# Optimization experiments

Hardware: AMD Instinct MI355X
Metric: run time of the kernel (lower is better)

The kernel has to match this reference:

```python
import jax, jax.numpy as jnp
import numpy as np

BN_EPS = 1e-5
N_SH, N_SS, N_HH, D = 1195, 390, 805, 64


def _gcn(x, edge_index, W, b, n_nodes, mean):
    # per-edge message = Linear(x_j); lin(x)[src] == lin(x[src])
    h = x @ W + b                                   # [N, out]
    msg = h[edge_index[0]]                          # gather sources -> [E, out]
    agg = jax.ops.segment_sum(msg, edge_index[1], num_segments=n_nodes)
    if mean:
        cnt = jax.ops.segment_sum(jnp.ones((edge_index.shape[1],), x.dtype),
                                  edge_index[1], num_segments=n_nodes)
        agg = agg / jnp.maximum(cnt, 1.0)[:, None]
    return jnp.tanh(agg)


def _bn(x, gamma, beta):
    # BatchNorm1d in training mode: biased batch statistics
    m = jnp.mean(x, axis=0)
    v = jnp.var(x, axis=0)
    return (x - m) * jax.lax.rsqrt(v + BN_EPS) * gamma + beta


def setup_inputs() -> dict:
    key = jax.random.key(0)
    ks = jax.random.split(key, 40)
    f32 = jnp.float32

    def lin(k, din, dout):
        k1, k2 = jax.random.split(k)
        s = 1.0 / np.sqrt(din)
        W = jax.random.uniform(k1, (din, dout), f32, -s, s)
        b = jax.random.uniform(k2, (dout,), f32, -s, s)
        return W, b

    inp = {}
    inp["x_SH"] = jnp.arange(N_SH, dtype=jnp.int64 if jax.config.jax_enable_x64 else jnp.int32)
    inp["edge_index_SH"] = jax.random.randint(ks[0], (2, 1_000_000), 0, N_SH)
    inp["x_SS"] = jnp.arange(N_SS)
    inp["edge_index_SS"] = jax.random.randint(ks[1], (2, 200_000), 0, N_SS)
    inp["x_HH"] = jnp.arange(N_HH)
    inp["edge_index_HH"] = jax.random.randint(ks[2], (2, 200_000), 0, N_HH)
    inp["prescription"] = jax.random.uniform(ks[3], (20000, N_SS), f32)
    inp["kgOneHot"] = jax.random.uniform(ks[4], (N_HH, 27), f32)

    inp["emb"] = jax.random.normal(ks[5], (N_SH, D), f32)
    inp["w_sh1"], inp["b_sh1"] = lin(ks[6], D, D)
    inp["w_sh2"], inp["b_sh2"] = lin(ks[7], D, D)
    inp["w_mlp1"], inp["b_mlp1"] = lin(ks[8], D, 256)
    inp["g_bn1"] = jnp.ones((256,), f32); inp["be_bn1"] = jnp.zeros((256,), f32)
    inp["w_sh1h"], inp["b_sh1h"] = lin(ks[9], D, D)
    inp["w_sh2h"], inp["b_sh2h"] = lin(ks[10], D, D)
    inp["w_mlp1h"], inp["b_mlp1h"] = lin(ks[11], D, 256)
    inp["g_bn1h"] = jnp.ones((256,), f32); inp["be_bn1h"] = jnp.zeros((256,), f32)
    inp["w_ss"], inp["b_ss"] = lin(ks[12], D, 256)
    inp["w_hh"], inp["b_hh"] = lin(ks[13], D + 27, 256)
    inp["w_mlp"], inp["b_mlp"] = lin(ks[14], 256, 256)
    inp["g_si"] = jnp.ones((256,), f32); inp["be_si"] = jnp.zeros((256,), f32)
    return inp


def reference(x_SH, edge_index_SH, x_SS, edge_index_SS, x_HH, edge_index_HH,
              prescription, kgOneHot, emb,
              w_sh1, b_sh1, w_sh2, b_sh2, w_mlp1, b_mlp1, g_bn1, be_bn1,
              w_sh1h, b_sh1h, w_sh2h, b_sh2h, w_mlp1h, b_mlp1h, g_bn1h, be_bn1h,
              w_ss, b_ss, w_hh, b_hh, w_mlp, b_mlp, g_si, be_si):
    # symptom branch on SH graph (mean aggregation)
    x1 = emb[x_SH]                                           # [1195, 64]
    x2 = _gcn(x1, edge_index_SH, w_sh1, b_sh1, N_SH, mean=True)
    x6 = _gcn(x2, edge_index_SH, w_sh2, b_sh2, N_SH, mean=True)
    x9 = (x1 + x2 + x6) / 3.0
    x9 = jnp.tanh(_bn(x9 @ w_mlp1 + b_mlp1, g_bn1, be_bn1))  # [1195, 256]

    # herb branch on SH graph
    x22 = _gcn(x1, edge_index_SH, w_sh1h, b_sh1h, N_SH, mean=True)
    x66 = _gcn(x22, edge_index_SH, w_sh2h, b_sh2h, N_SH, mean=True)
    x99 = (x1 + x22 + x66) / 3.0
    x99 = jnp.tanh(_bn(x99 @ w_mlp1h + b_mlp1h, g_bn1h, be_bn1h))

    # SS graph (add aggregation)
    x_ss1 = _gcn(emb[x_SS], edge_index_SS, w_ss, b_ss, N_SS, mean=False)  # [390, 256]

    # HH graph with KG one-hot features appended
    x_hh0 = jnp.concatenate([emb[x_HH], kgOneHot], axis=-1)  # [805, 91]
    x_hh1 = _gcn(x_hh0, edge_index_HH, w_hh, b_hh, N_HH, mean=False)      # [805, 256]

    es = x9[:N_SS] + x_ss1                                   # [390, 256]
    eh = x99[N_SS:] + x_hh1                                  # [805, 256]

    e_synd = prescription @ es                               # [B, 256]
    pre_sum = jnp.sum(prescription, axis=1, keepdims=True)
    e = e_synd / pre_sum
    e = jax.nn.relu(_bn(e @ w_mlp + b_mlp, g_si, be_si))
    return e @ eh.T                                          # [B, 805]
```

## Files before the change

kernel.cpp:

```cpp
#include <hip/hip_runtime.h>
#include <cstddef>
#include <cstdint>

#define N_SH 1195
#define N_SS 390
#define N_HH 805
#define DIM  64

typedef __bf16 bf16_t;
typedef bf16_t bf16x4v __attribute__((ext_vector_type(4)));
typedef bf16_t bf16x8v __attribute__((ext_vector_type(8)));
typedef float f32x4 __attribute__((ext_vector_type(4)));

__device__ inline ushort f2bf(float f) {
    union { float f; uint32_t u; } c; c.f = f;
    uint32_t u = c.u;
    u += 0x7FFFu + ((u >> 16) & 1u);
    return (ushort)(u >> 16);
}

__device__ inline void xcd_swizzle(int gx, int gy, int& bx, int& by) {
    int nwg = gx * gy;
    int lin = by * gx + bx;
    int q = nwg >> 3, r = nwg & 7;
    int xcd = lin & 7, idx = lin >> 3;
    int nt = (xcd < r ? xcd * (q + 1) : r * (q + 1) + (xcd - r) * q) + idx;
    by = nt / gx; bx = nt % gx;
}

__global__ void build_adj3_kernel(
    const int* __restrict__ e1, int E1, int hs1, uint32_t* __restrict__ T1,
    const int* __restrict__ e2, int E2, int hs2, uint32_t* __restrict__ T2,
    const int* __restrict__ e3, int E3, int hs3, uint32_t* __restrict__ T3)
{
    int i = blockIdx.x * blockDim.x + threadIdx.x;
    if (i < E1) {
        int src = e1[i], dst = e1[E1 + i];
        atomicAdd(&T1[(size_t)dst * hs1 + (src >> 2)], 1u << ((src & 3) * 8));
    } else if (i < E1 + E2) {
        int j = i - E1;
        int src = e2[j], dst = e2[E2 + j];
        atomicAdd(&T2[(size_t)dst * hs2 + (src >> 2)], 1u << ((src & 3) * 8));
    } else if (i < E1 + E2 + E3) {
        int j = i - E1 - E2;
        int src = e3[j], dst = e3[E3 + j];
        atomicAdd(&T3[(size_t)dst * hs3 + (src >> 2)], 1u << ((src & 3) * 8));
    }
}

__global__ void rowsum_inv_packed_kernel(const uint32_t* __restrict__ T, int R,
                                         int halfStride, float* __restrict__ inv) {
    int row  = blockIdx.x * (blockDim.x / 64) + (threadIdx.x / 64);
    int lane = threadIdx.x & 63;
    if (row >= R) return;
    const uint32_t* p = T + (size_t)row * halfStride;
    uint32_t s = 0;
    for (int c = lane; c < halfStride; c += 64) {
        uint32_t w = p[c];
        s += (w & 0xFFu) + ((w >> 8) & 0xFFu) + ((w >> 16) & 0xFFu) + (w >> 24);
    }
    for (int off = 32; off > 0; off >>= 1) s += __shfl_down(s, off);
    if (lane == 0) inv[row] = 1.0f / fmaxf((float)s, 1.0f);
}

__device__ inline void unpack_one(const uint32_t* __restrict__ T, int R, int C,
                                  int hs, ushort* __restrict__ out, int Cp, int i) {
    int r = i / Cp, c = i % Cp;
    float v = 0.f;
    if (r < R && c < C) {
        uint32_t w = T[(size_t)r * hs + (c >> 2)];
        v = (float)((w >> ((c & 3) * 8)) & 0xFFu);
    }
    out[i] = f2bf(v);
}

__global__ void cvt_unpack3_kernel(
    const uint32_t* __restrict__ T1, int hs1, ushort* __restrict__ o1, int n1, int Cp1,
    const uint32_t* __restrict__ T2, int hs2, ushort* __restrict__ o2, int n2, int Cp2,
    const uint32_t* __restrict__ T3, int hs3, ushort* __restrict__ o3, int n3, int Cp3)
{
    int i = blockIdx.x * blockDim.x + threadIdx.x;
    if (i < n1) { unpack_one(T1, N_SH, N_SH, hs1, o1, Cp1, i); return; }
    i -= n1;
    if (i < n2) { unpack_one(T2, N_SS, N_SS, hs2, o2, Cp2, i); return; }
    i -= n2;
    if (i < n3) { unpack_one(T3, N_HH, N_HH, hs3, o3, Cp3, i); }
}

#define BM 64
#define BN 64
#define BK 16

__global__ __launch_bounds__(256) void gemm_kernel(
    const float* __restrict__ A, const float* __restrict__ A2, int ldaA, int ldaA2,
    const float* __restrict__ B,
    const float* __restrict__ bias,
    float* __restrict__ C, ushort* __restrict__ outT, int ldt,
    int M, int N, int K, float* __restrict__ statsOut, int statsStride)
{
    __shared__ float As[BK][BM + 4];
    __shared__ float Bs[BK][BN];
    __shared__ float cs[128];
    const int tid  = threadIdx.x;
    const int row0 = blockIdx.y * BM;
    const int col0 = blockIdx.x * BN;
    const int tr  = (tid >> 4) << 2;
    const int tc  = (tid & 15) << 2;
    const int lar = tid >> 2;
    const int lac = (tid & 3) << 2;
    const int lbr = tid >> 4;
    const int lbc = (tid & 15) << 2;

    float acc[4][4] = {{0.f}};

    for (int k0 = 0; k0 < K; k0 += BK) {
        const int gr = row0 + lar;
        #pragma unroll
        for (int i = 0; i < 4; ++i) {
            int gk = k0 + lac + i;
            float v = 0.f;
            if (gr < M && gk < K) {
                v = A[(size_t)gr * ldaA + gk];
                if (A2) v += A2[(size_t)gr * ldaA2 + gk];
            }
            As[lac + i][lar] = v;
        }
        const int gk = k0 + lbr;
        const float* Bp = B + (size_t)gk * N + col0 + lbc;
        #pragma unroll
        for (int i = 0; i < 4; ++i) {
            int gc = col0 + lbc + i;
            Bs[lbr][lbc + i] = (gk < K && gc < N) ? Bp[i] : 0.f;
        }
        __syncthreads();
        #pragma unroll
        for (int kk = 0; kk < BK; ++kk) {
            float4 a = *reinterpret_cast<const float4*>(&As[kk][tr]);
            float4 b = *reinterpret_cast<const float4*>(&Bs[kk][tc]);
            acc[0][0] += a.x * b.x; acc[0][1] += a.x * b.y; acc[0][2] += a.x * b.z; acc[0][3] += a.x * b.w;
            acc[1][0] += a.y * b.x; acc[1][1] += a.y * b.y; acc[1][2] += a.y * b.z; acc[1][3] += a.y * b.w;
            acc[2][0] += a.z * b.x; acc[2][1] += a.z * b.y; acc[2][2] += a.z * b.z; acc[2][3] += a.z * b.w;
            acc[3][0] += a.w * b.x; acc[3][1] += a.w * b.y; acc[3][2] += a.w * b.z; acc[3][3] += a.w * b.w;
        }
        __syncthreads();
    }

    float ls[4] = {0.f, 0.f, 0.f, 0.f}, lq[4] = {0.f, 0.f, 0.f, 0.f};
    #pragma unroll
    for (int i = 0; i < 4; ++i) {
        int gr = row0 + tr + i;
        if (gr >= M) continue;
        #pragma unroll
        for (int j = 0; j < 4; ++j) {
            int gc = col0 + tc + j;
            if (gc >= N) continue;
            float v = acc[i][j];
            if (bias) v += bias[gc];
            if (outT) outT[(size_t)gc * ldt + gr] = f2bf(v);
            else      C[(size_t)gr * N + gc] = v;
            ls[j] += v; lq[j] += v * v;
        }
    }

    if (statsOut) {
        if (tid < 128) cs[tid] = 0.f;
        __syncthreads();
        #pragma unroll
        for (int j = 0; j < 4; ++j) {
            atomicAdd(&cs[tc + j], ls[j]);
            atomicAdd(&cs[64 + tc + j], lq[j]);
        }
        __syncthreads();
        if (tid < 64) {
            atomicAdd(&statsOut[col0 + tid], cs[tid]);
            atomicAdd(&statsOut[statsStride + col0 + tid], cs[64 + tid]);
        }
    }
}

#define LDT 40

__device__ inline void loadP8(const float* __restrict__ rowp, int c0, bool rv,
                              float* a, float& s) {
    if (rv && c0 + 8 <= N_SS) {
        float2 x0 = *reinterpret_cast<const float2*>(rowp + c0);
        float2 x1 = *reinterpret_cast<const float2*>(rowp + c0 + 2);
        float2 x2 = *reinterpret_cast<const float2*>(rowp + c0 + 4);
        float2 x3 = *reinterpret_cast<const float2*>(rowp + c0 + 6);
        a[0] = x0.x; a[1] = x0.y; a[2] = x1.x; a[3] = x1.y;
        a[4] = x2.x; a[5] = x2.y; a[6] = x3.x; a[7] = x3.y;
    } else {
        #pragma unroll
        for (int i = 0; i < 8; ++i) a[i] = (rv && (c0 + i) < N_SS) ? rowp[c0 + i] : 0.f;
    }
    #pragma unroll
    for (int i = 0; i < 8; ++i) s += a[i];
}

__global__ __launch_bounds__(256) void mfma_c1_kernel(
    const float* __restrict__ Pm, const ushort* __restrict__ Dt,
    int M, const float* __restrict__ bias,
    float* __restrict__ outF, float* __restrict__ statsOut)
{
    __shared__ __align__(16) ushort As[128 * LDT];
    __shared__ __align__(16) ushort Bs[128 * LDT];
    __shared__ float sums[128];
    __shared__ float cs[256];
    const int tid  = threadIdx.x;
    int bx = blockIdx.x, by = blockIdx.y;
    xcd_swizzle(gridDim.x, gridDim.y, bx, by);
    const int row0 = by * 128;
    const int col0 = bx * 128;
    const int wid  = tid >> 6, lane = tid & 63;
    const int wr = wid >> 1, wc = wid & 1;
    const int l15 = lane & 15, lg = lane >> 4;
    const int kg = lg * 4;
    const int sr = tid >> 2;
    const int sc = (tid & 3) * 8;

    const float* pA0 = Pm + (size_t)(row0 + sr)      * N_SS;
    const float* pA1 = Pm + (size_t)(row0 + sr + 64) * N_SS;
    const bool rv0 = (row0 + sr)      < M;
    const bool rv1 = (row0 + sr + 64) < M;
    const ushort* pB0 = Dt + (size_t)(col0 + sr)      * 416 + sc;
    const ushort* pB1 = Dt + (size_t)(col0 + sr + 64) * 416 + sc;

    float a0[8], a1[8];
    float s0 = 0.f, s1 = 0.f;
    loadP8(pA0, sc, rv0, a0, s0);
    loadP8(pA1, sc, rv1, a1, s1);
    uint4 b0 = *reinterpret_cast<const uint4*>(pB0);
    uint4 b1 = *reinterpret_cast<const uint4*>(pB1);

    f32x4 acc[4][4];
    #pragma unroll
    for (int m = 0; m < 4; ++m)
        #pragma unroll
        for (int n = 0; n < 4; ++n) acc[m][n] = (f32x4)0.f;

    for (int k0 = 0; k0 < 416; k0 += 32) {
        {
            bf16_t h[8];
            #pragma unroll
            for (int i = 0; i < 8; ++i) h[i] = (bf16_t)a0[i];
            *reinterpret_cast<uint4*>(&As[sr * LDT + sc]) = *reinterpret_cast<const uint4*>(h);
            #pragma unroll
            for (int i = 0; i < 8; ++i) h[i] = (bf16_t)a1[i];
            *reinterpret_cast<uint4*>(&As[(sr + 64) * LDT + sc]) = *reinterpret_cast<const uint4*>(h);
        }
        *reinterpret_cast<uint4*>(&Bs[sr * LDT + sc])        = b0;
        *reinterpret_cast<uint4*>(&Bs[(sr + 64) * LDT + sc]) = b1;
        __syncthreads();
        if (k0 + 32 < 416) {
            loadP8(pA0, k0 + 32 + sc, rv0, a0, s0);
            loadP8(pA1, k0 + 32 + sc, rv1, a1, s1);
            b0 = *reinterpret_cast<const uint4*>(pB0 + k0 + 32);
            b1 = *reinterpret_cast<const uint4*>(pB1 + k0 + 32);
        }

        bf16x8v af[4], bfr[4];
        #pragma unroll
        for (int m = 0; m < 4; ++m) {
            int ar = wr * 64 + m * 16 + l15;
            bf16x4v lo = *reinterpret_cast<const bf16x4v*>(&As[ar * LDT + kg]);
            bf16x4v hi = *reinterpret_cast<const bf16x4v*>(&As[ar * LDT + kg + 16]);
            af[m] = __builtin_shufflevector(lo, hi, 0, 1, 2, 3, 4, 5, 6, 7);
        }
        #pragma unroll
        for (int n = 0; n < 4; ++n) {
            int br = wc * 64 + n * 16 + l15;
            bf16x4v lo = *reinterpret_cast<const bf16x4v*>(&Bs[br * LDT + kg]);
            bf16x4v hi = *reinterpret_cast<const bf16x4v*>(&Bs[br * LDT + kg + 16]);
            bfr[n] = __builtin_shufflevector(lo, hi, 0, 1, 2, 3, 4, 5, 6, 7);
        }
        #pragma unroll
        for (int m = 0; m < 4; ++m)
            #pragma unroll
            for (int n = 0; n < 4; ++n)
                acc[m][n] = __builtin_amdgcn_mfma_f32_16x16x32_bf16(af[m], bfr[n], acc[m][n], 0, 0, 0);
        __syncthreads();
    }

    if (tid < 128) sums[tid] = 0.f;
    if (tid < 256) cs[tid] = 0.f;
    __syncthreads();
    atomicAdd(&sums[sr], s0);
    atomicAdd(&sums[sr + 64], s1);
    __syncthreads();

    float ls[4] = {0.f, 0.f, 0.f, 0.f}, lq[4] = {0.f, 0.f, 0.f, 0.f};
    #pragma unroll
    for (int m = 0; m < 4; ++m) {
        int lr_base = wr * 64 + m * 16 + kg;
        #pragma unroll
        for (int j = 0; j < 4; ++j) {
            int lr = lr_base + j;
            int grow = row0 + lr;
            if (grow >= M) continue;
            float t = sums[lr];
            float inv = (t != 0.f) ? 1.0f / t : 0.f;
            #pragma unroll
            for (int n = 0; n < 4; ++n) {
                int gcol = col0 + wc * 64 + n * 16 + l15;
                float v = acc[m][n][j] * inv + bias[gcol];
                outF[(size_t)grow * 256 + gcol] = v;
                ls[n] += v; lq[n] += v * v;
            }
        }
    }

    __syncthreads();
    #pragma unroll
    for (int n = 0; n < 4; ++n) {
        int lc = wc * 64 + n * 16 + l15;
        atomicAdd(&cs[lc], ls[n]);
        atomicAdd(&cs[128 + lc], lq[n]);
    }
    __syncthreads();
    if (tid < 128) {
        atomicAdd(&statsOut[col0 + tid], cs[tid]);
        atomicAdd(&statsOut[256 + col0 + tid], cs[128 + tid]);
    }
}

__global__ __launch_bounds__(256) void mfma_c3_kernel(
    const float* __restrict__ Abuf, const ushort* __restrict__ Bt,
    int M, int Nw,
    const float* __restrict__ stats, const float* __restrict__ g,
    const float* __restrict__ be,
    float* __restrict__ outF, int ldo)
{
    __shared__ __align__(16) ushort As[128 * LDT];
    __shared__ __align__(16) ushort Bs[128 * LDT];
    __shared__ float sscale[256], sshift[256];
    const int tid  = threadIdx.x;
    int bx = blockIdx.x, by = blockIdx.y;
    xcd_swizzle(gridDim.x, gridDim.y, bx, by);
    const int row0 = by * 128;
    const int col0 = bx * 128;
    const int wid  = tid >> 6, lane = tid & 63;
    const int wr = wid >> 1, wc = wid & 1;
    const int l15 = lane & 15, lg = lane >> 4;
    const int kg = lg * 4;
    const int sr = tid >> 2;
    const int sc = (tid & 3) * 8;

    if (tid < 256) {
        float invM = 1.0f / (float)M;
        float mean = stats[tid] * invM;
        float var  = fmaxf(stats[256 + tid] * invM - mean * mean, 0.f);
        float scv  = g[tid] * rsqrtf(var + 1e-5f);
        sscale[tid] = scv;
        sshift[tid] = be[tid] - mean * scv;
    }
    __syncthreads();

    const float*  pA0 = Abuf + (size_t)(row0 + sr)      * 256 + sc;
    const float*  pA1 = Abuf + (size_t)(row0 + sr + 64) * 256 + sc;
    const ushort* pB0 = Bt + (size_t)(col0 + sr)        * 256 + sc;
    const ushort* pB1 = Bt + (size_t)(col0 + sr + 64)   * 256 + sc;

    float4 a00 = *reinterpret_cast<const float4*>(pA0);
    float4 a01 = *reinterpret_cast<const float4*>(pA0 + 4);
    float4 a10 = *reinterpret_cast<const float4*>(pA1);
    float4 a11 = *reinterpret_cast<const float4*>(pA1 + 4);
    uint4  b0  = *reinterpret_cast<const uint4*>(pB0);
    uint4  b1  = *reinterpret_cast<const uint4*>(pB1);

    f32x4 acc[4][4];
    #pragma unroll
    for (int m = 0; m < 4; ++m)
        #pragma unroll
        for (int n = 0; n < 4; ++n) acc[m][n] = (f32x4)0.f;

    for (int k0 = 0; k0 < 256; k0 += 32) {
        float s8[8], t8[8];
        #pragma unroll
        for (int i = 0; i < 8; ++i) { s8[i] = sscale[k0 + sc + i]; t8[i] = sshift[k0 + sc + i]; }
        {
            bf16_t h[8];
            h[0] = (bf16_t)fmaxf(a00.x * s8[0] + t8[0], 0.f);
            h[1] = (bf16_t)fmaxf(a00.y * s8[1] + t8[1], 0.f);
            h[2] = (bf16_t)fmaxf(a00.z * s8[2] + t8[2], 0.f);
            h[3] = (bf16_t)fmaxf(a00.w * s8[3] + t8[3], 0.f);
            h[4] = (bf16_t)fmaxf(a01.x * s8[4] + t8[4], 0.f);
            h[5] = (bf16_t)fmaxf(a01.y * s8[5] + t8[5], 0.f);
            h[6] = (bf16_t)fmaxf(a01.z * s8[6] + t8[6], 0.f);
            h[7] = (bf16_t)fmaxf(a01.w * s8[7] + t8[7], 0.f);
            *reinterpret_cast<uint4*>(&As[sr * LDT + sc]) = *reinterpret_cast<const uint4*>(h);
            h[0] = (bf16_t)fmaxf(a10.x * s8[0] + t8[0], 0.f);
            h[1] = (bf16_t)fmaxf(a10.y * s8[1] + t8[1], 0.f);
            h[2] = (bf16_t)fmaxf(a10.z * s8[2] + t8[2], 0.f);
            h[3] = (bf16_t)fmaxf(a10.w * s8[3] + t8[3], 0.f);
            h[4] = (bf16_t)fmaxf(a11.x * s8[4] + t8[4], 0.f);
            h[5] = (bf16_t)fmaxf(a11.y * s8[5] + t8[5], 0.f);
            h[6] = (bf16_t)fmaxf(a11.z * s8[6] + t8[6], 0.f);
            h[7] = (bf16_t)fmaxf(a11.w * s8[7] + t8[7], 0.f);
            *reinterpret_cast<uint4*>(&As[(sr + 64) * LDT + sc]) = *reinterpret_cast<const uint4*>(h);
        }
        *reinterpret_cast<uint4*>(&Bs[sr * LDT + sc])        = b0;
        *reinterpret_cast<uint4*>(&Bs[(sr + 64) * LDT + sc]) = b1;
        __syncthreads();
        if (k0 + 32 < 256) {
            a00 = *reinterpret_cast<const float4*>(pA0 + k0 + 32);
            a01 = *reinterpret_cast<const float4*>(pA0 + k0 + 36);
            a10 = *reinterpret_cast<const float4*>(pA1 + k0 + 32);
            a11 = *reinterpret_cast<const float4*>(pA1 + k0 + 36);
            b0  = *reinterpret_cast<const uint4*>(pB0 + k0 + 32);
            b1  = *reinterpret_cast<const uint4*>(pB1 + k0 + 32);
        }

        bf16x8v af[4], bfr[4];
        #pragma unroll
        for (int m = 0; m < 4; ++m) {
            int ar = wr * 64 + m * 16 + l15;
            bf16x4v lo = *reinterpret_cast<const bf16x4v*>(&As[ar * LDT + kg]);
            bf16x4v hi = *reinterpret_cast<const bf16x4v*>(&As[ar * LDT + kg + 16]);
            af[m] = __builtin_shufflevector(lo, hi, 0, 1, 2, 3, 4, 5, 6, 7);
        }
        #pragma unroll
        for (int n = 0; n < 4; ++n) {
            int br = wc * 64 + n * 16 + l15;
            bf16x4v lo = *reinterpret_cast<const bf16x4v*>(&Bs[br * LDT + kg]);
            bf16x4v hi = *reinterpret_cast<const bf16x4v*>(&Bs[br * LDT + kg + 16]);
            bfr[n] = __builtin_shufflevector(lo, hi, 0, 1, 2, 3, 4, 5, 6, 7);
        }
        #pragma unroll
        for (int m = 0; m < 4; ++m)
            #pragma unroll
            for (int n = 0; n < 4; ++n)
                acc[m][n] = __builtin_amdgcn_mfma_f32_16x16x32_bf16(af[m], bfr[n], acc[m][n], 0, 0, 0);
        __syncthreads();
    }

    #pragma unroll
    for (int m = 0; m < 4; ++m) {
        int grow_base = row0 + wr * 64 + m * 16 + kg;
        #pragma unroll
        for (int j = 0; j < 4; ++j) {
            int grow = grow_base + j;
            if (grow >= M) continue;
            #pragma unroll
            for (int n = 0; n < 4; ++n) {
                int gcol = col0 + wc * 64 + n * 16 + l15;
                if (gcol >= Nw) continue;
                outF[(size_t)grow * ldo + gcol] = acc[m][n][j];
            }
        }
    }
}

__global__ __launch_bounds__(256) void mfma_splitk_kernel(
    const ushort* __restrict__ A, const ushort* __restrict__ Bt,
    int M, int K, int lda, int kChunk, int Ntot,
    float* __restrict__ part)
{
    __shared__ __align__(16) ushort As[128 * LDT];
    __shared__ __align__(16) ushort Bs[128 * LDT];
    const int tid  = threadIdx.x;
    const int row0 = blockIdx.y * 128;
    const int col0 = blockIdx.x * 128;
    const int wid  = tid >> 6, lane = tid & 63;
    const int wr = wid >> 1, wc = wid & 1;
    const int l15 = lane & 15, lg = lane >> 4;
    const int kg = lg * 4;
    const int sr = tid >> 2;
    const int sc = (tid & 3) * 8;

    const int k0s = blockIdx.z * kChunk;
    const int k0e = (k0s + kChunk < K) ? k0s + kChunk : K;

    const ushort* pA0 = A  + (size_t)(row0 + sr)      * lda + sc;
    const ushort* pA1 = A  + (size_t)(row0 + sr + 64) * lda + sc;
    const ushort* pB0 = Bt + (size_t)(col0 + sr)      * lda + sc;
    const ushort* pB1 = Bt + (size_t)(col0 + sr + 64) * lda + sc;

    uint4 ra0 = *reinterpret_cast<const uint4*>(pA0 + k0s);
    uint4 ra1 = *reinterpret_cast<const uint4*>(pA1 + k0s);
    uint4 rb0 = *reinterpret_cast<const uint4*>(pB0 + k0s);
    uint4 rb1 = *reinterpret_cast<const uint4*>(pB1 + k0s);

    f32x4 acc[4][4];
    #pragma unroll
    for (int m = 0; m < 4; ++m)
        #pragma unroll
        for (int n = 0; n < 4; ++n) acc[m][n] = (f32x4)0.f;

    for (int k0 = k0s; k0 < k0e; k0 += 32) {
        *reinterpret_cast<uint4*>(&As[sr * LDT + sc])        = ra0;
        *reinterpret_cast<uint4*>(&As[(sr + 64) * LDT + sc]) = ra1;
        *reinterpret_cast<uint4*>(&Bs[sr * LDT + sc])        = rb0;
        *reinterpret_cast<uint4*>(&Bs[(sr + 64) * LDT + sc]) = rb1;
        __syncthreads();
        if (k0 + 32 < k0e) {
            ra0 = *reinterpret_cast<const uint4*>(pA0 + k0 + 32);
            ra1 = *reinterpret_cast<const uint4*>(pA1 + k0 + 32);
            rb0 = *reinterpret_cast<const uint4*>(pB0 + k0 + 32);
            rb1 = *reinterpret_cast<const uint4*>(pB1 + k0 + 32);
        }

        bf16x8v af[4], bfr[4];
        #pragma unroll
        for (int m = 0; m < 4; ++m) {
            int ar = wr * 64 + m * 16 + l15;
            bf16x4v lo = *reinterpret_cast<const bf16x4v*>(&As[ar * LDT + kg]);
            bf16x4v hi = *reinterpret_cast<const bf16x4v*>(&As[ar * LDT + kg + 16]);
            af[m] = __builtin_shufflevector(lo, hi, 0, 1, 2, 3, 4, 5, 6, 7);
        }
        #pragma unroll
        for (int n = 0; n < 4; ++n) {
            int br = wc * 64 + n * 16 + l15;
            bf16x4v lo = *reinterpret_cast<const bf16x4v*>(&Bs[br * LDT + kg]);
            bf16x4v hi = *reinterpret_cast<const bf16x4v*>(&Bs[br * LDT + kg + 16]);
            bfr[n] = __builtin_shufflevector(lo, hi, 0, 1, 2, 3, 4, 5, 6, 7);
        }
        #pragma unroll
        for (int m = 0; m < 4; ++m)
            #pragma unroll
            for (int n = 0; n < 4; ++n)
                acc[m][n] = __builtin_amdgcn_mfma_f32_16x16x32_bf16(af[m], bfr[n], acc[m][n], 0, 0, 0);
        __syncthreads();
    }

    float* pslab = part + (size_t)blockIdx.z * M * Ntot;
    #pragma unroll
    for (int m = 0; m < 4; ++m) {
        int grow_base = row0 + wr * 64 + m * 16 + kg;
        #pragma unroll
        for (int j = 0; j < 4; ++j) {
            int grow = grow_base + j;
            if (grow >= M) continue;
            #pragma unroll
            for (int n = 0; n < 4; ++n) {
                int gcol = col0 + wc * 64 + n * 16 + l15;
                pslab[(size_t)grow * Ntot + gcol] = acc[m][n][j];
            }
        }
    }
}

__global__ void reduce_tanh_kernel(const float* __restrict__ part, int S, int M, int N,
                                   const float* __restrict__ rs,
                                   const float* __restrict__ emb,
                                   const float* __restrict__ prev,
                                   float* __restrict__ out) {
    int i = blockIdx.x * blockDim.x + threadIdx.x;
    if (i >= M * N) return;
    int r = i / N, j = i - r * N;
    float s = 0.f;
    for (int z = 0; z < S; ++z) s += part[(size_t)z * M * N + i];
    if (rs) s *= rs[r];
    float t = tanhf(s);
    if (emb) out[i] = (emb[r * 64 + (j & 63)] + prev[i] + t) * (1.0f / 3.0f);
    else     out[i] = t;
}

__global__ void make_cat_weights_kernel(
    const float* __restrict__ w_sh1, const float* __restrict__ w_sh1h,
    const float* __restrict__ b_sh1, const float* __restrict__ b_sh1h,
    const float* __restrict__ w_sh2, const float* __restrict__ w_sh2h,
    const float* __restrict__ b_sh2, const float* __restrict__ b_sh2h,
    const float* __restrict__ w_mlp1, const float* __restrict__ w_mlp1h,
    const float* __restrict__ b_mlp1, const float* __restrict__ b_mlp1h,
    float* __restrict__ W1cat, float* __restrict__ b1cat,
    float* __restrict__ W2bd,  float* __restrict__ b2cat,
    float* __restrict__ WMbd,  float* __restrict__ bMcat)
{
    int i = blockIdx.x * blockDim.x + threadIdx.x;
    if (i < 64 * 128) {
        int k = i >> 7, j = i & 127;
        W1cat[i] = (j < 64) ? w_sh1[k * 64 + j] : w_sh1h[k * 64 + (j - 64)];
        return;
    }
    i -= 64 * 128;
    if (i < 128) { b1cat[i] = (i < 64) ? b_sh1[i] : b_sh1h[i - 64]; return; }
    i -= 128;
    if (i < 128 * 128) {
        int k = i >> 7, j = i & 127;
        float v = 0.f;
        if (k < 64 && j < 64) v = w_sh2[k * 64 + j];
        else if (k >= 64 && j >= 64) v = w_sh2h[(k - 64) * 64 + (j - 64)];
        W2bd[i] = v;
        return;
    }
    i -= 128 * 128;
    if (i < 128) { b2cat[i] = (i < 64) ? b_sh2[i] : b_sh2h[i - 64]; return; }
    i -= 128;
    if (i < 128 * 512) {
        int k = i >> 9, j = i & 511;
        float v = 0.f;
        if (j < 256) { if (k < 64) v = w_mlp1[k * 256 + j]; }
        else         { if (k >= 64) v = w_mlp1h[(k - 64) * 256 + (j - 256)]; }
        WMbd[i] = v;
        return;
    }
    i -= 128 * 512;
    if (i < 512) { bMcat[i] = (i < 256) ? b_mlp1[i] : b_mlp1h[i - 256]; }
}

__global__ void concat_hh_kernel(const float* __restrict__ emb, const float* __restrict__ kg,
                                 float* __restrict__ out) {
    int i = blockIdx.x * blockDim.x + threadIdx.x;
    const int n = N_HH * 91;
    if (i >= n) return;
    int r = i / 91, c = i % 91;
    out[i] = (c < DIM) ? emb[r * DIM + c] : kg[r * 27 + (c - DIM)];
}

__global__ void make_ehb_kernel(const float* __restrict__ x9cat, const float* __restrict__ hh1,
                                ushort* __restrict__ out, int Rp) {
    int i = blockIdx.x * blockDim.x + threadIdx.x;
    if (i >= Rp * 256) return;
    int r = i >> 8, c = i & 255;
    float v = (r < N_HH) ? (x9cat[(size_t)(N_SS + r) * 512 + 256 + c] + hh1[(size_t)r * 256 + c]) : 0.f;
    out[i] = f2bf(v);
}

__global__ void bn_apply_cat_kernel(const float* __restrict__ X, const float* __restrict__ stats,
                                    const float* __restrict__ g1, const float* __restrict__ be1,
                                    const float* __restrict__ g2, const float* __restrict__ be2,
                                    int M, float* __restrict__ out) {
    int i = blockIdx.x * blockDim.x + threadIdx.x;
    if (i >= M * 512) return;
    int j = i & 511;
    float invM = 1.0f / (float)M;
    float mean = stats[j] * invM;
    float var  = fmaxf(stats[512 + j] * invM - mean * mean, 0.f);
    float ga = (j < 256) ? g1[j]  : g2[j - 256];
    float bb = (j < 256) ? be1[j] : be2[j - 256];
    float y = (X[i] - mean) * rsqrtf(var + 1e-5f) * ga + bb;
    out[i] = tanhf(y);
}

extern "C" void kernel_launch(void* const* d_in, const int* in_sizes, int n_in,
                              void* d_out, int out_size, void* d_ws, size_t ws_size,
                              hipStream_t stream) {
    const int*   eiSH = (const int*)d_in[1];
    const int*   eiSS = (const int*)d_in[3];
    const int*   eiHH = (const int*)d_in[5];
    const float* P    = (const float*)d_in[6];
    const float* kg   = (const float*)d_in[7];
    const float* emb  = (const float*)d_in[8];
    const float* w_sh1  = (const float*)d_in[9];   const float* b_sh1  = (const float*)d_in[10];
    const float* w_sh2  = (const float*)d_in[11];  const float* b_sh2  = (const float*)d_in[12];
    const float* w_mlp1 = (const float*)d_in[13];  const float* b_mlp1 = (const float*)d_in[14];
    const float* g_bn1  = (const float*)d_in[15];  const float* be_bn1 = (const float*)d_in[16];
    const float* w_sh1h = (const float*)d_in[17];  const float* b_sh1h = (const float*)d_in[18];
    const float* w_sh2h = (const float*)d_in[19];  const float* b_sh2h = (const float*)d_in[20];
    const float* w_mlp1h= (const float*)d_in[21];  const float* b_mlp1h= (const float*)d_in[22];
    const float* g_bn1h = (const float*)d_in[23];  const float* be_bn1h= (const float*)d_in[24];
    const float* w_ss   = (const float*)d_in[25];  const float* b_ss   = (const float*)d_in[26];
    const float* w_hh   = (const float*)d_in[27];  const float* b_hh   = (const float*)d_in[28];
    const float* w_mlp  = (const float*)d_in[29];  const float* b_mlp  = (const float*)d_in[30];
    const float* g_si   = (const float*)d_in[31];  const float* be_si  = (const float*)d_in[32];
    float* out = (float*)d_out;

    const int E_SH = in_sizes[1] / 2;
    const int E_SS = in_sizes[3] / 2;
    const int E_HH = in_sizes[5] / 2;
    const int B    = in_sizes[6] / N_SS;
    const int Mp   = ((B + 127) / 128) * 128;
    const int KP1  = 416;
    const int NP3  = 896;
    const int KSH  = 1216;
    const int KHH  = 832;
    const int HS_SH = (N_SH + 3) / 4;
    const int HS_SS = (N_SS + 3) / 4;
    const int HS_HH = (N_HH + 3) / 4;

    float* w = (float*)d_ws;
    size_t off = 0;
    auto alloc = [&](size_t n) { float* p = w + off; off += (n + 3) & ~(size_t)3; return p; };

    float* cntInv   = alloc(N_SH);
    float* statsCat = alloc(1024);
    float* statsC2  = alloc(512);
    ushort* HT      = (ushort*)alloc((size_t)128 * KSH / 2);
    ushort* HSST    = (ushort*)alloc((size_t)256 * KP1 / 2);
    ushort* HHHT    = (ushort*)alloc((size_t)256 * KHH / 2);
    ushort* eswT    = (ushort*)alloc((size_t)256 * KP1 / 2);
    float* zeroEnd  = w + off;
    float* W1cat   = alloc(64 * 128);
    float* b1cat   = alloc(128);
    float* W2bd    = alloc(128 * 128);
    float* b2cat   = alloc(128);
    float* WMbd    = alloc(128 * 512);
    float* bMcat   = alloc(512);
    ushort* adjb   = (ushort*)alloc((size_t)1280 * KSH / 2);
    ushort* adjSSb = (ushort*)alloc((size_t)512 * KP1 / 2);
    ushort* adjHHb = (ushort*)alloc((size_t)896 * KHH / 2);
    float* x2cat   = alloc((size_t)N_SH * 128);
    float* x9a2    = alloc((size_t)N_SH * 128);
    float* tmpBN   = alloc((size_t)N_SH * 512);
    float* x9cat   = alloc((size_t)N_SH * 512);
    float* ss1     = alloc((size_t)N_SS * 256);
    float* hh1     = alloc((size_t)N_HH * 256);
    float* xhh0    = alloc((size_t)N_HH * 91);
    ushort* eh_b   = (ushort*)alloc((size_t)NP3 * 256 / 2);
    float* regionA = alloc((size_t)Mp * 256);
    uint32_t* uSH  = (uint32_t*)regionA;
    uint32_t* uSS  = uSH + (size_t)N_SH * HS_SH;
    uint32_t* uHH  = uSS + (size_t)N_SS * HS_SS;
    size_t packed_words = (size_t)N_SH * HS_SH + (size_t)N_SS * HS_SS + (size_t)N_HH * HS_HH;
    float*  bufM   = regionA;
    float* regionB = alloc((size_t)Mp * 256);
    float*  partials = regionB;
    (void)ws_size; (void)n_in; (void)out_size;

    auto gemmT = [&](const float* Am, const float* A2m, int lda1, int lda2,
                     const float* Bm, const float* bias,
                     ushort* oT, int ldt, int M, int N, int K) {
        dim3 g((N + BN - 1) / BN, (M + BM - 1) / BM);
        gemm_kernel<<<g, 256, 0, stream>>>(Am, A2m, lda1, lda2, Bm, bias,
                                           nullptr, oT, ldt, M, N, K, nullptr, 0);
    };
    auto gemmF = [&](const float* Am, const float* Bm, const float* bias,
                     float* C, int M, int N, int K, float* st, int sstride) {
        dim3 g((N + BN - 1) / BN, (M + BM - 1) / BM);
        gemm_kernel<<<g, 256, 0, stream>>>(Am, nullptr, K, 0, Bm, bias,
                                           C, nullptr, 0, M, N, K, st, sstride);
    };
    auto splitk = [&](const ushort* Am, const ushort* Bm, int M, int Mtiles, int K, int lda,
                      int Ntot, int S, const float* rs, const float* embA, const float* prev,
                      float* outp) {
        dim3 g(Ntot / 128, Mtiles, S);
        mfma_splitk_kernel<<<g, 256, 0, stream>>>(Am, Bm, M, K, lda, 128, Ntot, partials);
        reduce_tanh_kernel<<<(M * Ntot + 255) / 256, 256, 0, stream>>>(
            partials, S, M, Ntot, rs, embA, prev, outp);
    };

    hipMemsetAsync(uSH, 0, packed_words * sizeof(uint32_t), stream);
    hipMemsetAsync(statsCat, 0, (size_t)((char*)zeroEnd - (char*)statsCat), stream);

    {
        int Etot = E_SH + E_SS + E_HH;
        build_adj3_kernel<<<(Etot + 255) / 256, 256, 0, stream>>>(
            eiSH, E_SH, HS_SH, uSH, eiSS, E_SS, HS_SS, uSS, eiHH, E_HH, HS_HH, uHH);
    }
    rowsum_inv_packed_kernel<<<(N_SH + 3) / 4, 256, 0, stream>>>(uSH, N_SH, HS_SH, cntInv);
    {
        int n1 = 1280 * KSH, n2 = 512 * KP1, n3 = 896 * KHH;
        cvt_unpack3_kernel<<<(n1 + n2 + n3 + 255) / 256, 256, 0, stream>>>(
            uSH, HS_SH, adjb, n1, KSH, uSS, HS_SS, adjSSb, n2, KP1, uHH, HS_HH, adjHHb, n3, KHH);
    }

    make_cat_weights_kernel<<<(90880 + 255) / 256, 256, 0, stream>>>(
        w_sh1, w_sh1h, b_sh1, b_sh1h, w_sh2, w_sh2h, b_sh2, b_sh2h,
        w_mlp1, w_mlp1h, b_mlp1, b_mlp1h,
        W1cat, b1cat, W2bd, b2cat, WMbd, bMcat);

    gemmT(emb, nullptr, 64, 0, W1cat, b1cat, HT, KSH, N_SH, 128, 64);
    splitk(adjb, HT, N_SH, 10, KSH, KSH, 128, 10, cntInv, nullptr, nullptr, x2cat);
    gemmT(x2cat, nullptr, 128, 0, W2bd, b2cat, HT, KSH, N_SH, 128, 128);
    splitk(adjb, HT, N_SH, 10, KSH, KSH, 128, 10, cntInv, emb, x2cat, x9a2);
    gemmF(x9a2, WMbd, bMcat, tmpBN, N_SH, 512, 128, statsCat, 512);
    bn_apply_cat_kernel<<<(N_SH * 512 + 255) / 256, 256, 0, stream>>>(
        tmpBN, statsCat, g_bn1, be_bn1, g_bn1h, be_bn1h, N_SH, x9cat);

    gemmT(emb, nullptr, 64, 0, w_ss, b_ss, HSST, KP1, N_SS, 256, 64);
    splitk(adjSSb, HSST, N_SS, 4, KP1, KP1, 256, 4, nullptr, nullptr, nullptr, ss1);

    concat_hh_kernel<<<(N_HH * 91 + 255) / 256, 256, 0, stream>>>(emb, kg, xhh0);
    gemmT(xhh0, nullptr, 91, 0, w_hh, b_hh, HHHT, KHH, N_HH, 256, 91);
    splitk(adjHHb, HHHT, N_HH, 7, KHH, KHH, 256, 7, nullptr, nullptr, nullptr, hh1);

    make_ehb_kernel<<<(NP3 * 256 + 255) / 256, 256, 0, stream>>>(x9cat, hh1, eh_b, NP3);

    gemmT(x9cat, ss1, 512, 256, w_mlp, nullptr, eswT, KP1, N_SS, 256, 256);
    {
        dim3 g(2, (B + 127) / 128);
        mfma_c1_kernel<<<g, 256, 0, stream>>>(P, eswT, B, b_mlp, bufM, statsC2);
    }
    {
        dim3 g(NP3 / 128, (B + 127) / 128);
        mfma_c3_kernel<<<g, 256, 0, stream>>>(bufM, eh_b, B, N_HH, statsC2, g_si, be_si, out, N_HH);
    }
}
```

Before: 315.3 us.

## Merge prep kernels into one launch and fuse BN+tanh into consumers

Folds the row-sum inverse, adjacency unpack, weight concatenation and HH feature concat kernels into a single mega prep kernel, which cuts the number of small launches. It also removes the standalone batch-norm apply kernel. BN+tanh is now applied on the fly, inside the GEMM's A-load for the first 256 columns and inside the eh construction kernel for the herb half, so the full x9cat buffer is never written or read. The trade-off is redundant tanh work per GEMM tile and a branchier prep kernel.

```diff
diff --git a/kernel.cpp b/kernel.cpp
--- a/kernel.cpp
+++ b/kernel.cpp
@@ -48,21 +48,6 @@
     }
 }
 
-__global__ void rowsum_inv_packed_kernel(const uint32_t* __restrict__ T, int R,
-                                         int halfStride, float* __restrict__ inv) {
-    int row  = blockIdx.x * (blockDim.x / 64) + (threadIdx.x / 64);
-    int lane = threadIdx.x & 63;
-    if (row >= R) return;
-    const uint32_t* p = T + (size_t)row * halfStride;
-    uint32_t s = 0;
-    for (int c = lane; c < halfStride; c += 64) {
-        uint32_t w = p[c];
-        s += (w & 0xFFu) + ((w >> 8) & 0xFFu) + ((w >> 16) & 0xFFu) + (w >> 24);
-    }
-    for (int off = 32; off > 0; off >>= 1) s += __shfl_down(s, off);
-    if (lane == 0) inv[row] = 1.0f / fmaxf((float)s, 1.0f);
-}
-
 __device__ inline void unpack_one(const uint32_t* __restrict__ T, int R, int C,
                                   int hs, ushort* __restrict__ out, int Cp, int i) {
     int r = i / Cp, c = i % Cp;
@@ -74,17 +59,77 @@
     out[i] = f2bf(v);
 }
 
-__global__ void cvt_unpack3_kernel(
+__global__ void mega_prep_kernel(
     const uint32_t* __restrict__ T1, int hs1, ushort* __restrict__ o1, int n1, int Cp1,
     const uint32_t* __restrict__ T2, int hs2, ushort* __restrict__ o2, int n2, int Cp2,
-    const uint32_t* __restrict__ T3, int hs3, ushort* __restrict__ o3, int n3, int Cp3)
+    const uint32_t* __restrict__ T3, int hs3, ushort* __restrict__ o3, int n3, int Cp3,
+    float* __restrict__ cntInv,
+    const float* __restrict__ w_sh1, const float* __restrict__ w_sh1h,
+    const float* __restrict__ b_sh1, const float* __restrict__ b_sh1h,
+    const float* __restrict__ w_sh2, const float* __restrict__ w_sh2h,
+    const float* __restrict__ b_sh2, const float* __restrict__ b_sh2h,
+    const float* __restrict__ w_mlp1, const float* __restrict__ w_mlp1h,
+    const float* __restrict__ b_mlp1, const float* __restrict__ b_mlp1h,
+    float* __restrict__ W1cat, float* __restrict__ b1cat,
+    float* __restrict__ W2bd,  float* __restrict__ b2cat,
+    float* __restrict__ WMbd,  float* __restrict__ bMcat,
+    const float* __restrict__ emb, const float* __restrict__ kg,
+    float* __restrict__ xhh0)
 {
     int i = blockIdx.x * blockDim.x + threadIdx.x;
     if (i < n1) { unpack_one(T1, N_SH, N_SH, hs1, o1, Cp1, i); return; }
     i -= n1;
     if (i < n2) { unpack_one(T2, N_SS, N_SS, hs2, o2, Cp2, i); return; }
     i -= n2;
-    if (i < n3) { unpack_one(T3, N_HH, N_HH, hs3, o3, Cp3, i); }
+    if (i < n3) { unpack_one(T3, N_HH, N_HH, hs3, o3, Cp3, i); return; }
+    i -= n3;
+    if (i < N_SH * 64) {
+        int row = i >> 6, lane = i & 63;
+        const uint32_t* p = T1 + (size_t)row * hs1;
+        uint32_t s = 0;
+        for (int c = lane; c < hs1; c += 64) {
+            uint32_t w0 = p[c];
+            s += (w0 & 0xFFu) + ((w0 >> 8) & 0xFFu) + ((w0 >> 16) & 0xFFu) + (w0 >> 24);
+        }
+        for (int off = 32; off > 0; off >>= 1) s += __shfl_down(s, off);
+        if (lane == 0) cntInv[row] = 1.0f / fmaxf((float)s, 1.0f);
+        return;
+    }
+    i -= N_SH * 64;
+    if (i < 64 * 128) {
+        int k = i >> 7, j = i & 127;
+        W1cat[i] = (j < 64) ? w_sh1[k * 64 + j] : w_sh1h[k * 64 + (j - 64)];
+        return;
+    }
+    i -= 64 * 128;
+    if (i < 128) { b1cat[i] = (i < 64) ? b_sh1[i] : b_sh1h[i - 64]; return; }
+    i -= 128;
+    if (i < 128 * 128) {
+        int k = i >> 7, j = i & 127;
+        float v = 0.f;
+        if (k < 64 && j < 64) v = w_sh2[k * 64 + j];
+        else if (k >= 64 && j >= 64) v = w_sh2h[(k - 64) * 64 + (j - 64)];
+        W2bd[i] = v;
+        return;
+    }
+    i -= 128 * 128;
+    if (i < 128) { b2cat[i] = (i < 64) ? b_sh2[i] : b_sh2h[i - 64]; return; }
+    i -= 128;
+    if (i < 128 * 512) {
+        int k = i >> 9, j = i & 511;
+        float v = 0.f;
+        if (j < 256) { if (k < 64) v = w_mlp1[k * 256 + j]; }
+        else         { if (k >= 64) v = w_mlp1h[(k - 64) * 256 + (j - 256)]; }
+        WMbd[i] = v;
+        return;
+    }
+    i -= 128 * 512;
+    if (i < 512) { bMcat[i] = (i < 256) ? b_mlp1[i] : b_mlp1h[i - 256]; return; }
+    i -= 512;
+    if (i < N_HH * 91) {
+        int r = i / 91, c = i % 91;
+        xhh0[i] = (c < DIM) ? emb[r * DIM + c] : kg[r * 27 + (c - DIM)];
+    }
 }
 
 #define BM 64
@@ -96,11 +141,14 @@
     const float* __restrict__ B,
     const float* __restrict__ bias,
     float* __restrict__ C, ushort* __restrict__ outT, int ldt,
-    int M, int N, int K, float* __restrict__ statsOut, int statsStride)
+    int M, int N, int K, float* __restrict__ statsOut, int statsStride,
+    const float* __restrict__ bnStats, const float* __restrict__ bnG,
+    const float* __restrict__ bnBe, int bnM)
 {
     __shared__ float As[BK][BM + 4];
     __shared__ float Bs[BK][BN];
     __shared__ float cs[128];
+    __shared__ float sA[256], tA[256];
     const int tid  = threadIdx.x;
     const int row0 = blockIdx.y * BM;
     const int col0 = blockIdx.x * BN;
@@ -111,6 +159,16 @@
     const int lbr = tid >> 4;
     const int lbc = (tid & 15) << 2;
 
+    if (bnStats) {
+        float invM = 1.0f / (float)bnM;
+        float mean = bnStats[tid] * invM;
+        float var  = fmaxf(bnStats[512 + tid] * invM - mean * mean, 0.f);
+        float scv  = bnG[tid] * rsqrtf(var + 1e-5f);
+        sA[tid] = scv;
+        tA[tid] = bnBe[tid] - mean * scv;
+        __syncthreads();
+    }
+
     float acc[4][4] = {{0.f}};
 
     for (int k0 = 0; k0 < K; k0 += BK) {
@@ -121,6 +179,7 @@
             float v = 0.f;
             if (gr < M && gk < K) {
                 v = A[(size_t)gr * ldaA + gk];
+                if (bnStats) v = tanhf(v * sA[gk] + tA[gk]);
                 if (A2) v += A2[(size_t)gr * ldaA2 + gk];
             }
             As[lac + i][lar] = v;
@@ -555,81 +614,25 @@
     else     out[i] = t;
 }
 
-__global__ void make_cat_weights_kernel(
-    const float* __restrict__ w_sh1, const float* __restrict__ w_sh1h,
-    const float* __restrict__ b_sh1, const float* __restrict__ b_sh1h,
-    const float* __restrict__ w_sh2, const float* __restrict__ w_sh2h,
-    const float* __restrict__ b_sh2, const float* __restrict__ b_sh2h,
-    const float* __restrict__ w_mlp1, const float* __restrict__ w_mlp1h,
-    const float* __restrict__ b_mlp1, const float* __restrict__ b_mlp1h,
-    float* __restrict__ W1cat, float* __restrict__ b1cat,
-    float* __restrict__ W2bd,  float* __restrict__ b2cat,
-    float* __restrict__ WMbd,  float* __restrict__ bMcat)
-{
-    int i = blockIdx.x * blockDim.x + threadIdx.x;
-    if (i < 64 * 128) {
-        int k = i >> 7, j = i & 127;
-        W1cat[i] = (j < 64) ? w_sh1[k * 64 + j] : w_sh1h[k * 64 + (j - 64)];
-        return;
-    }
-    i -= 64 * 128;
-    if (i < 128) { b1cat[i] = (i < 64) ? b_sh1[i] : b_sh1h[i - 64]; return; }
-    i -= 128;
-    if (i < 128 * 128) {
-        int k = i >> 7, j = i & 127;
-        float v = 0.f;
-        if (k < 64 && j < 64) v = w_sh2[k * 64 + j];
-        else if (k >= 64 && j >= 64) v = w_sh2h[(k - 64) * 64 + (j - 64)];
-        W2bd[i] = v;
-        return;
-    }
-    i -= 128 * 128;
-    if (i < 128) { b2cat[i] = (i < 64) ? b_sh2[i] : b_sh2h[i - 64]; return; }
-    i -= 128;
-    if (i < 128 * 512) {
-        int k = i >> 9, j = i & 511;
-        float v = 0.f;
-        if (j < 256) { if (k < 64) v = w_mlp1[k * 256 + j]; }
-        else         { if (k >= 64) v = w_mlp1h[(k - 64) * 256 + (j - 256)]; }
-        WMbd[i] = v;
-        return;
-    }
-    i -= 128 * 512;
-    if (i < 512) { bMcat[i] = (i < 256) ? b_mlp1[i] : b_mlp1h[i - 256]; }
-}
-
-__global__ void concat_hh_kernel(const float* __restrict__ emb, const float* __restrict__ kg,
-                                 float* __restrict__ out) {
-    int i = blockIdx.x * blockDim.x + threadIdx.x;
-    const int n = N_HH * 91;
-    if (i >= n) return;
-    int r = i / 91, c = i % 91;
-    out[i] = (c < DIM) ? emb[r * DIM + c] : kg[r * 27 + (c - DIM)];
-}
-
-__global__ void make_ehb_kernel(const float* __restrict__ x9cat, const float* __restrict__ hh1,
-                                ushort* __restrict__ out, int Rp) {
+__global__ void make_ehb_bn_kernel(const float* __restrict__ tmpBN,
+                                   const float* __restrict__ stats,
+                                   const float* __restrict__ g, const float* __restrict__ be,
+                                   const float* __restrict__ hh1,
+                                   ushort* __restrict__ out, int Rp) {
     int i = blockIdx.x * blockDim.x + threadIdx.x;
     if (i >= Rp * 256) return;
     int r = i >> 8, c = i & 255;
-    float v = (r < N_HH) ? (x9cat[(size_t)(N_SS + r) * 512 + 256 + c] + hh1[(size_t)r * 256 + c]) : 0.f;
+    float v = 0.f;
+    if (r < N_HH) {
+        float invM = 1.0f / (float)N_SH;
+        int j = 256 + c;
+        float mean = stats[j] * invM;
+        float var  = fmaxf(stats[512 + j] * invM - mean * mean, 0.f);
+        float x = tmpBN[(size_t)(N_SS + r) * 512 + j];
+        float y = tanhf((x - mean) * rsqrtf(var + 1e-5f) * g[c] + be[c]);
+        v = y + hh1[(size_t)r * 256 + c];
+    }
     out[i] = f2bf(v);
-}
-
-__global__ void bn_apply_cat_kernel(const float* __restrict__ X, const float* __restrict__ stats,
-                                    const float* __restrict__ g1, const float* __restrict__ be1,
-                                    const float* __restrict__ g2, const float* __restrict__ be2,
-                                    int M, float* __restrict__ out) {
-    int i = blockIdx.x * blockDim.x + threadIdx.x;
-    if (i >= M * 512) return;
-    int j = i & 511;
-    float invM = 1.0f / (float)M;
-    float mean = stats[j] * invM;
-    float var  = fmaxf(stats[512 + j] * invM - mean * mean, 0.f);
-    float ga = (j < 256) ? g1[j]  : g2[j - 256];
-    float bb = (j < 256) ? be1[j] : be2[j - 256];
-    float y = (X[i] - mean) * rsqrtf(var + 1e-5f) * ga + bb;
-    out[i] = tanhf(y);
 }
 
 extern "C" void kernel_launch(void* const* d_in, const int* in_sizes, int n_in,
@@ -692,7 +695,6 @@
     float* x2cat   = alloc((size_t)N_SH * 128);
     float* x9a2    = alloc((size_t)N_SH * 128);
     float* tmpBN   = alloc((size_t)N_SH * 512);
-    float* x9cat   = alloc((size_t)N_SH * 512);
     float* ss1     = alloc((size_t)N_SS * 256);
     float* hh1     = alloc((size_t)N_HH * 256);
     float* xhh0    = alloc((size_t)N_HH * 91);
@@ -709,16 +711,19 @@
 
     auto gemmT = [&](const float* Am, const float* A2m, int lda1, int lda2,
                      const float* Bm, const float* bias,
-                     ushort* oT, int ldt, int M, int N, int K) {
+                     ushort* oT, int ldt, int M, int N, int K,
+                     const float* bnS, const float* bnG, const float* bnB, int bnM) {
         dim3 g((N + BN - 1) / BN, (M + BM - 1) / BM);
         gemm_kernel<<<g, 256, 0, stream>>>(Am, A2m, lda1, lda2, Bm, bias,
-                                           nullptr, oT, ldt, M, N, K, nullptr, 0);
+                                           nullptr, oT, ldt, M, N, K, nullptr, 0,
+                                           bnS, bnG, bnB, bnM);
     };
     auto gemmF = [&](const float* Am, const float* Bm, const float* bias,
                      float* C, int M, int N, int K, float* st, int sstride) {
         dim3 g((N + BN - 1) / BN, (M + BM - 1) / BM);
         gemm_kernel<<<g, 256, 0, stream>>>(Am, nullptr, K, 0, Bm, bias,
-                                           C, nullptr, 0, M, N, K, st, sstride);
+                                           C, nullptr, 0, M, N, K, st, sstride,
+                                           nullptr, nullptr, nullptr, 0);
     };
     auto splitk = [&](const ushort* Am, const ushort* Bm, int M, int Mtiles, int K, int lda,
                       int Ntot, int S, const float* rs, const float* embA, const float* prev,
@@ -737,36 +742,39 @@
         build_adj3_kernel<<<(Etot + 255) / 256, 256, 0, stream>>>(
             eiSH, E_SH, HS_SH, uSH, eiSS, E_SS, HS_SS, uSS, eiHH, E_HH, HS_HH, uHH);
     }
-    rowsum_inv_packed_kernel<<<(N_SH + 3) / 4, 256, 0, stream>>>(uSH, N_SH, HS_SH, cntInv);
     {
         int n1 = 1280 * KSH, n2 = 512 * KP1, n3 = 896 * KHH;
-        cvt_unpack3_kernel<<<(n1 + n2 + n3 + 255) / 256, 256, 0, stream>>>(
-            uSH, HS_SH, adjb, n1, KSH, uSS, HS_SS, adjSSb, n2, KP1, uHH, HS_HH, adjHHb, n3, KHH);
-    }
-
-    make_cat_weights_kernel<<<(90880 + 255) / 256, 256, 0, stream>>>(
-        w_sh1, w_sh1h, b_sh1, b_sh1h, w_sh2, w_sh2h, b_sh2, b_sh2h,
-        w_mlp1, w_mlp1h, b_mlp1, b_mlp1h,
-        W1cat, b1cat, W2bd, b2cat, WMbd, bMcat);
-
-    gemmT(emb, nullptr, 64, 0, W1cat, b1cat, HT, KSH, N_SH, 128, 64);
+        int tot = n1 + n2 + n3 + N_SH * 64 + 90880 + N_HH * 91;
+        mega_prep_kernel<<<(tot + 255) / 256, 256, 0, stream>>>(
+            uSH, HS_SH, adjb, n1, KSH, uSS, HS_SS, adjSSb, n2, KP1,
+            uHH, HS_HH, adjHHb, n3, KHH, cntInv,
+            w_sh1, w_sh1h, b_sh1, b_sh1h, w_sh2, w_sh2h, b_sh2, b_sh2h,
+            w_mlp1, w_mlp1h, b_mlp1, b_mlp1h,
+            W1cat, b1cat, W2bd, b2cat, WMbd, bMcat,
+            emb, kg, xhh0);
+    }
+
+    gemmT(emb, nullptr, 64, 0, W1cat, b1cat, HT, KSH, N_SH, 128, 64,
+          nullptr, nullptr, nullptr, 0);
     splitk(adjb, HT, N_SH, 10, KSH, KSH, 128, 10, cntInv, nullptr, nullptr, x2cat);
-    gemmT(x2cat, nullptr, 128, 0, W2bd, b2cat, HT, KSH, N_SH, 128, 128);
+    gemmT(x2cat, nullptr, 128, 0, W2bd, b2cat, HT, KSH, N_SH, 128, 128,
+          nullptr, nullptr, nullptr, 0);
     splitk(adjb, HT, N_SH, 10, KSH, KSH, 128, 10, cntInv, emb, x2cat, x9a2);
     gemmF(x9a2, WMbd, bMcat, tmpBN, N_SH, 512, 128, statsCat, 512);
-    bn_apply_cat_kernel<<<(N_SH * 512 + 255) / 256, 256, 0, stream>>>(
-        tmpBN, statsCat, g_bn1, be_bn1, g_bn1h, be_bn1h, N_SH, x9cat);
-
-    gemmT(emb, nullptr, 64, 0, w_ss, b_ss, HSST, KP1, N_SS, 256, 64);
+
+    gemmT(emb, nullptr, 64, 0, w_ss, b_ss, HSST, KP1, N_SS, 256, 64,
+          nullptr, nullptr, nullptr, 0);
     splitk(adjSSb, HSST, N_SS, 4, KP1, KP1, 256, 4, nullptr, nullptr, nullptr, ss1);
 
-    concat_hh_kernel<<<(N_HH * 91 + 255) / 256, 256, 0, stream>>>(emb, kg, xhh0);
-    gemmT(xhh0, nullptr, 91, 0, w_hh, b_hh, HHHT, KHH, N_HH, 256, 91);
+    gemmT(xhh0, nullptr, 91, 0, w_hh, b_hh, HHHT, KHH, N_HH, 256, 91,
+          nullptr, nullptr, nullptr, 0);
     splitk(adjHHb, HHHT, N_HH, 7, KHH, KHH, 256, 7, nullptr, nullptr, nullptr, hh1);
 
-    make_ehb_kernel<<<(NP3 * 256 + 255) / 256, 256, 0, stream>>>(x9cat, hh1, eh_b, NP3);
-
-    gemmT(x9cat, ss1, 512, 256, w_mlp, nullptr, eswT, KP1, N_SS, 256, 256);
+    make_ehb_bn_kernel<<<(NP3 * 256 + 255) / 256, 256, 0, stream>>>(
+        tmpBN, statsCat, g_bn1h, be_bn1h, hh1, eh_b, NP3);
+
+    gemmT(tmpBN, ss1, 512, 256, w_mlp, nullptr, eswT, KP1, N_SS, 256, 256,
+          statsCat, g_bn1, be_bn1, N_SH);
     {
         dim3 g(2, (B + 127) / 128);
         mfma_c1_kernel<<<g, 256, 0, stream>>>(P, eswT, B, b_mlp, bufM, statsC2);
```

Result: no change. 318.3 us (+0.9%).
